# Optimization experiments

Hardware: AMD Instinct MI355X
Metric: run time of the kernel (lower is better)

## Reference

```python
import jax, jax.numpy as jnp
import numpy as np
import math

HEADS = 8


def rope(t):
    # t: [..., seq, dim]; lucidrains-style interleaved rotary embedding
    seq, dim = t.shape[-2], t.shape[-1]
    inv = 1.0 / (10000.0 ** (jnp.arange(0, dim, 2, dtype=jnp.float32) / dim))
    freqs = jnp.arange(seq, dtype=jnp.float32)[:, None] * inv[None, :]  # [seq, dim/2]
    freqs = jnp.repeat(freqs, 2, axis=-1)                               # [seq, dim]
    cos, sin = jnp.cos(freqs), jnp.sin(freqs)
    t2 = t.reshape(t.shape[:-1] + (dim // 2, 2))
    rot = jnp.stack([-t2[..., 1], t2[..., 0]], axis=-1).reshape(t.shape)
    return t * cos + rot * sin


def conv1x3(x, w):
    # x: [b,c,h,w], w: [out_c,in_c,1,3], padding (0,1), no bias
    return jax.lax.conv_general_dilated(
        x, w, window_strides=(1, 1), padding=((0, 0), (1, 1)),
        dimension_numbers=('NCHW', 'OIHW', 'NCHW'))


def mcl_pw(x, w_pw):
    # per-channel linear on feature axis h: w_pw [c, out_f, in_f]
    return jnp.einsum('bchw,cgh->bcgw', x, w_pw)


def setup_inputs() -> dict:
    key = jax.random.key(0)
    ks = jax.random.split(key, 10)
    b, c, f, w = 2, 8, 256, 1024
    s = 0.05
    return {
        'x': jax.random.normal(ks[0], (b, c, f, w), dtype=jnp.float32),
        'q_pw': jax.random.normal(ks[1], (c, f, f), dtype=jnp.float32) * s,
        'q_cw': jax.random.normal(ks[2], (c, c, 1, 3), dtype=jnp.float32) * s,
        'k_pw': jax.random.normal(ks[3], (c, f, f), dtype=jnp.float32) * s,
        'k_cw': jax.random.normal(ks[4], (c, c, 1, 3), dtype=jnp.float32) * s,
        'v_pw': jax.random.normal(ks[5], (c, f, f), dtype=jnp.float32) * s,
        'v_cw': jax.random.normal(ks[6], (c, c, 1, 3), dtype=jnp.float32) * s,
        'out_pw': jax.random.normal(ks[7], (c, f, f), dtype=jnp.float32) * s,
        'out_dw': jax.random.normal(ks[8], (c, c), dtype=jnp.float32) * s,
    }


def reference(x, q_pw, q_cw, k_pw, k_cw, v_pw, v_cw, out_pw, out_dw):
    b, c, h, w = x.shape
    hd = h // HEADS

    def split_heads(y):  # [b,c,h,w] -> [b,c,heads,w,hd]
        return y.transpose(0, 1, 3, 2).reshape(b, c, w, HEADS, hd).transpose(0, 1, 3, 2, 4)

    q = rope(split_heads(conv1x3(mcl_pw(x, q_pw), q_cw)))
    k = rope(split_heads(conv1x3(mcl_pw(x, k_pw), k_cw)))
    v = split_heads(conv1x3(mcl_pw(x, v_pw), v_cw))

    # non-standard scaling by sqrt(h) = sqrt(features)
    qk = jnp.einsum('bcnqd,bcnkd->bcnqk', q, k) / math.sqrt(h)
    a = jnp.einsum('bcnqk,bcnkd->bcnqd', jax.nn.softmax(qk, axis=-1), v)
    a = a.transpose(0, 1, 3, 2, 4).reshape(b, c, w, h).transpose(0, 1, 3, 2)  # [b,c,h,w]

    # out_proj: depthwise channel mix then per-channel positionwise linear
    out = jnp.einsum('bchw,dc->bdhw', a, out_dw)
    out = mcl_pw(out, out_pw)
    return out
```

## Files before the change

### kernel.cpp

```cpp
#include <hip/hip_runtime.h>
#include <hip/hip_bf16.h>

#define B 2
#define C 8
#define F 256
#define W 1024
#define NH 8
#define HD 32

typedef float f32x4 __attribute__((ext_vector_type(4)));
typedef short sh8 __attribute__((ext_vector_type(8)));
typedef short sh4 __attribute__((ext_vector_type(4)));
typedef unsigned short u16;

#define QSCALE 0.09016843880556021f

static __device__ __forceinline__ float fexp2(float x) {
#if __has_builtin(__builtin_amdgcn_exp2f)
  return __builtin_amdgcn_exp2f(x);
#else
  return __expf(x * 0.69314718056f);
#endif
}

static __device__ __forceinline__ u16 f2b(float x) {
  union { __hip_bfloat16 h; u16 u; } v;
  v.h = __float2bfloat16(x);
  return v.u;
}
static __device__ __forceinline__ float b2f(u16 x) {
  union { unsigned int u; float f; } v;
  v.u = ((unsigned int)x) << 16;
  return v.f;
}
static __device__ __forceinline__ float ubits(unsigned int u) {
  union { unsigned int u; float f; } v;
  v.u = u;
  return v.f;
}

static __device__ __forceinline__ f32x4 mfma32(sh8 a, sh8 b, f32x4 c) {
  return __builtin_amdgcn_mfma_f32_16x16x32_bf16(a, b, c, 0, 0, 0);
}

static __device__ __forceinline__ f32x4 mfma16(sh4 a, sh4 b, f32x4 c) {
#if __has_builtin(__builtin_amdgcn_mfma_f32_16x16x16bf16_1k)
  return __builtin_amdgcn_mfma_f32_16x16x16bf16_1k(a, b, c, 0, 0, 0);
#else
  f32x4 d;
  asm("v_mfma_f32_16x16x16_bf16 %0, %1, %2, %3" : "=v"(d) : "v"(a), "v"(b), "v"(c));
  return d;
#endif
}

static __device__ __forceinline__ void gload16(const u16* g, u16* l, int ln) {
#if __has_builtin(__builtin_amdgcn_global_load_lds)
  __builtin_amdgcn_global_load_lds((const __attribute__((address_space(1))) void*)g,
                                   (__attribute__((address_space(3))) void*)l, 16, 0, 0);
#else
  *(sh8*)(l + ln * 8) = *(const sh8*)g;
#endif
}

__global__ __launch_bounds__(256) void cvt4(const float* __restrict__ s0, const float* __restrict__ s1,
                                            const float* __restrict__ s2, const float* __restrict__ s3,
                                            u16* __restrict__ d0, u16* __restrict__ d1,
                                            u16* __restrict__ d2, u16* __restrict__ d3, int n4) {
  const int which = blockIdx.y;
  const float* s = which == 0 ? s0 : which == 1 ? s1 : which == 2 ? s2 : s3;
  u16* d = which == 0 ? d0 : which == 1 ? d1 : which == 2 ? d2 : d3;
  const int i = blockIdx.x * 256 + threadIdx.x;
  if (i < n4) {
    const float4 v = reinterpret_cast<const float4*>(s)[i];
    union { u16 h[4]; uint2 u; } o;
    o.h[0] = f2b(v.x); o.h[1] = f2b(v.y); o.h[2] = f2b(v.z); o.h[3] = f2b(v.w);
    reinterpret_cast<uint2*>(d)[i] = o.u;
  }
}

__global__ __launch_bounds__(256) void rope_tab_k(float2* __restrict__ TAB) {
  const int idx = blockIdx.x * 256 + threadIdx.x;
  const int j = idx >> 10, w = idx & 1023;
  const float inv = powf(10000.f, -(float)(2 * j) / 32.f);
  float sn, cs;
  sincosf((float)w * inv, &sn, &cs);
  TAB[idx] = make_float2(cs, sn);
}

__global__ __launch_bounds__(256) void xt_k(const float* __restrict__ x,
                                            u16* __restrict__ xt) {
  const int bc = blockIdx.z, h0 = blockIdx.y * 32, w0 = blockIdx.x * 32;
  const int t = threadIdx.x;
  __shared__ u16 sm[32][34];
  const int a = t & 31, bql = t >> 5;
  const float* src = x + ((size_t)bc * F + h0) * W + w0;
#pragma unroll
  for (int p = 0; p < 4; ++p) {
    const int hl = bql + p * 8;
    sm[a][hl] = f2b(src[(size_t)hl * W + a]);
  }
  __syncthreads();
  u16* dst = xt + ((size_t)bc * W + w0) * F + h0;
#pragma unroll
  for (int p = 0; p < 4; ++p) {
    const int wl = bql + p * 8;
    dst[(size_t)wl * F + a] = sm[wl][a];
  }
}

template <bool OUTBF>
__global__ __launch_bounds__(256) void gemm_bt(const u16* __restrict__ Aw,
                                               const u16* __restrict__ Bt,
                                               void* __restrict__ Cc) {
  const int bc = blockIdx.z;
  const int proj = blockIdx.y >> 1;
  const int g0 = (blockIdx.y & 1) * 128;
  const int w0 = blockIdx.x * 64;
  const int t = threadIdx.x;
  const int ln = t & 63, wid = t >> 6;
  const int lr = ln & 15, lk = (ln >> 4) * 8;
  const int wr = wid >> 1, wc = wid & 1;

  const u16* Ab = Aw + (size_t)proj * C * F * F + (size_t)(bc & 7) * F * F;
  const u16* Bb = Bt + (size_t)bc * W * F;

  __shared__ u16 sA[16 * 512];
  __shared__ u16 sB[8 * 512];

  const u16* ga0 = Ab + (size_t)(g0 + (wid * 2 + 0) * 16 + lr) * F + lk;
  const u16* ga1 = Ab + (size_t)(g0 + (wid * 2 + 1) * 16 + lr) * F + lk;
  const u16* gb0 = Bb + (size_t)(w0 + wid * 16 + lr) * F + lk;

  f32x4 acc[4][2] = {};

  for (int h0 = 0; h0 < F; h0 += 64) {
    __syncthreads();
    gload16(ga0 + h0,      &sA[(0 * 8 + wid * 2 + 0) * 512], ln);
    gload16(ga0 + h0 + 32, &sA[(1 * 8 + wid * 2 + 0) * 512], ln);
    gload16(ga1 + h0,      &sA[(0 * 8 + wid * 2 + 1) * 512], ln);
    gload16(ga1 + h0 + 32, &sA[(1 * 8 + wid * 2 + 1) * 512], ln);
    gload16(gb0 + h0,      &sB[(0 * 4 + wid) * 512], ln);
    gload16(gb0 + h0 + 32, &sB[(1 * 4 + wid) * 512], ln);
    __syncthreads();
#pragma unroll
    for (int kh = 0; kh < 2; ++kh) {
      sh8 af[4], bfr[2];
#pragma unroll
      for (int mi = 0; mi < 4; ++mi)
        af[mi] = *(const sh8*)&sA[((kh * 8 + wr * 4 + mi) * 64 + ln) * 8];
#pragma unroll
      for (int ni = 0; ni < 2; ++ni)
        bfr[ni] = *(const sh8*)&sB[((kh * 4 + wc * 2 + ni) * 64 + ln) * 8];
#pragma unroll
      for (int mi = 0; mi < 4; ++mi)
#pragma unroll
        for (int ni = 0; ni < 2; ++ni)
          acc[mi][ni] = mfma32(af[mi], bfr[ni], acc[mi][ni]);
    }
  }

  const int lq = ln >> 4;
  const size_t cbase = ((size_t)proj * B * C + bc) * F * W;
  if (OUTBF) {
    u16* Cb = (u16*)Cc + cbase;
#pragma unroll
    for (int mi = 0; mi < 4; ++mi)
#pragma unroll
      for (int ni = 0; ni < 2; ++ni)
#pragma unroll
        for (int r = 0; r < 4; ++r)
          Cb[(size_t)(g0 + wr * 64 + mi * 16 + lq * 4 + r) * W + w0 + wc * 32 + ni * 16 + lr] =
              f2b(acc[mi][ni][r]);
  } else {
    float* Cb = (float*)Cc + cbase;
#pragma unroll
    for (int mi = 0; mi < 4; ++mi)
#pragma unroll
      for (int ni = 0; ni < 2; ++ni)
#pragma unroll
        for (int r = 0; r < 4; ++r)
          Cb[(size_t)(g0 + wr * 64 + mi * 16 + lq * 4 + r) * W + w0 + wc * 32 + ni * 16 + lr] =
              acc[mi][ni][r];
  }
}

__global__ __launch_bounds__(256) void conv2(const u16* __restrict__ IN,
                                             const float* __restrict__ CWq,
                                             const float* __restrict__ CWk,
                                             const float* __restrict__ CWv,
                                             const float* __restrict__ TAB,
                                             u16* __restrict__ OUT) {
  const int f2 = blockIdx.x;
  const int z = blockIdx.y;
  const int proj = z >> 1, b = z & 1;
  const float* CW = proj == 0 ? CWq : proj == 1 ? CWk : CWv;
  const size_t NB = (size_t)B * C * F * W;
  const u16* INp = IN + (size_t)proj * NB;
  u16* OUTp = OUT + (size_t)proj * NB;
  const int do_rope = (proj < 2);
  const float scale = (proj == 0) ? QSCALE : 1.0f;
  const int f0 = f2 * 2;
  const int t = threadIdx.x;

  __shared__ u16 s[2][C][1040];
  __shared__ float cw[C][C][3];
  if (t < C * C * 3) ((float*)cw)[t] = CW[t];
  if (t < 16) {
    const int fi = t >> 3, c2 = t & 7;
    s[fi][c2][7] = 0;
    s[fi][c2][1032] = 0;
  }
  {
    const int l = t & 127, rsel = t >> 7;
#pragma unroll
    for (int p = 0; p < 8; ++p) {
      const int row = p * 2 + rsel;
      const int fi = row >> 3, c2 = row & 7;
      const u16* src = INp + ((size_t)(b * C + c2) * F + f0 + fi) * W + l * 8;
      *(sh8*)&s[fi][c2][8 + l * 8] = *(const sh8*)src;
    }
  }
  __syncthreads();

  float acc[2][C][4] = {};
#pragma unroll
  for (int c = 0; c < C; ++c) {
    float v[2][6];
#pragma unroll
    for (int fi = 0; fi < 2; ++fi) {
      const unsigned int* r32 = (const unsigned int*)&s[fi][c][0];
      const unsigned int r0 = r32[2 * t + 3];
      const unsigned int r1 = r32[2 * t + 4];
      const unsigned int r2 = r32[2 * t + 5];
      const unsigned int r3 = r32[2 * t + 6];
      v[fi][0] = ubits(r0 & 0xffff0000u);
      v[fi][1] = ubits(r1 << 16);
      v[fi][2] = ubits(r1 & 0xffff0000u);
      v[fi][3] = ubits(r2 << 16);
      v[fi][4] = ubits(r2 & 0xffff0000u);
      v[fi][5] = ubits(r3 << 16);
    }
#pragma unroll
    for (int d = 0; d < C; ++d) {
      const float c0 = cw[d][c][0], c1 = cw[d][c][1], c2_ = cw[d][c][2];
#pragma unroll
      for (int fi = 0; fi < 2; ++fi)
#pragma unroll
        for (int o = 0; o < 4; ++o)
          acc[fi][d][o] += v[fi][o] * c0 + v[fi][o + 1] * c1 + v[fi][o + 2] * c2_;
    }
  }

  float cs[4] = {1.f, 1.f, 1.f, 1.f}, sn[4] = {0.f, 0.f, 0.f, 0.f};
  if (do_rope) {
    const int j = f2 & 15;
    const float4* tp = (const float4*)(TAB + (size_t)(j * 1024 + 4 * t) * 2);
    const float4 A0 = tp[0], A1 = tp[1];
    cs[0] = A0.x; sn[0] = A0.y; cs[1] = A0.z; sn[1] = A0.w;
    cs[2] = A1.x; sn[2] = A1.y; cs[3] = A1.z; sn[3] = A1.w;
  }

#pragma unroll
  for (int d = 0; d < C; ++d) {
    sh4 pk0, pk1;
#pragma unroll
    for (int o = 0; o < 4; ++o) {
      const float a0 = acc[0][d][o], a1 = acc[1][d][o];
      float o0 = a0, o1 = a1;
      if (do_rope) { o0 = a0 * cs[o] - a1 * sn[o]; o1 = a1 * cs[o] + a0 * sn[o]; }
      pk0[o] = (short)f2b(o0 * scale);
      pk1[o] = (short)f2b(o1 * scale);
    }
    u16* dst = OUTp + ((size_t)(b * C + d) * F + f0) * W + 4 * t;
    *(sh4*)dst = pk0;
    *(sh4*)(dst + W) = pk1;
  }
}

__global__ __launch_bounds__(256) void attn_bf(const u16* __restrict__ Q,
                                               const u16* __restrict__ K,
                                               const u16* __restrict__ Vv,
                                               float* __restrict__ O) {
  const int bc = blockIdx.z, n = blockIdx.y, q0 = blockIdx.x * 64;
  const int t = threadIdx.x, ln = t & 63, wid = t >> 6;
  const int lc = ln & 15, g4 = (ln >> 4) * 4;
  const int dq = (ln >> 4) * 8;
  const size_t base = ((size_t)bc * F + n * HD) * W;

  __shared__ u16 Kl[2][64 * 40];
  __shared__ u16 Vl[2][32 * 76];

  const int sk = t & 63, sdb = (t >> 6) * 8;
  const int sd = t >> 3, skc = (t & 7) * 8;
  const u16* gK = K + base + (size_t)sdb * W + sk;
  const u16* gV = Vv + base + (size_t)sd * W + skc;

  const int qw = q0 + wid * 16 + lc;
  sh8 qf;
#pragma unroll
  for (int j = 0; j < 8; ++j) qf[j] = (short)Q[base + (size_t)(dq + j) * W + qw];

  f32x4 o0 = {0.f, 0.f, 0.f, 0.f}, o1 = {0.f, 0.f, 0.f, 0.f};
  float ls[4] = {0.f, 0.f, 0.f, 0.f};

  {
    sh8 hv;
#pragma unroll
    for (int j = 0; j < 8; ++j) hv[j] = (short)gK[(size_t)j * W];
    *(sh8*)&Kl[0][sk * 40 + sdb] = hv;
    *(sh8*)&Vl[0][sd * 76 + skc] = *(const sh8*)gV;
  }
  __syncthreads();

  for (int tile = 0; tile < 16; ++tile) {
    const int cur = tile & 1;
    sh8 hvK, hvV;
    if (tile < 15) {
      const int off = (tile + 1) * 64;
#pragma unroll
      for (int j = 0; j < 8; ++j) hvK[j] = (short)gK[(size_t)j * W + off];
      hvV = *(const sh8*)(gV + off);
    }

    f32x4 sf[4];
    __builtin_amdgcn_s_setprio(1);
#pragma unroll
    for (int kh = 0; kh < 4; ++kh) {
      const sh8 kf = *(const sh8*)&Kl[cur][(kh * 16 + lc) * 40 + dq];
      f32x4 z = {0.f, 0.f, 0.f, 0.f};
      sf[kh] = mfma32(kf, qf, z);
    }
    __builtin_amdgcn_s_setprio(0);

#pragma unroll
    for (int kh = 0; kh < 4; ++kh) {
      const float p0 = fexp2(sf[kh][0]);
      const float p1 = fexp2(sf[kh][1]);
      const float p2 = fexp2(sf[kh][2]);
      const float p3 = fexp2(sf[kh][3]);
      sf[kh][0] = p0; sf[kh][1] = p1; sf[kh][2] = p2; sf[kh][3] = p3;
      ls[kh] += (p0 + p1) + (p2 + p3);
    }

    __builtin_amdgcn_s_setprio(1);
#pragma unroll
    for (int kh = 0; kh < 4; ++kh) {
      const sh4 pb = {(short)f2b(sf[kh][0]), (short)f2b(sf[kh][1]),
                      (short)f2b(sf[kh][2]), (short)f2b(sf[kh][3])};
      const sh4 vf0 = *(const sh4*)&Vl[cur][lc * 76 + kh * 16 + g4];
      const sh4 vf1 = *(const sh4*)&Vl[cur][(16 + lc) * 76 + kh * 16 + g4];
      o0 = mfma16(pb, vf0, o0);
      o1 = mfma16(pb, vf1, o1);
    }
    __builtin_amdgcn_s_setprio(0);

    if (tile < 15) {
      *(sh8*)&Kl[cur ^ 1][sk * 40 + sdb] = hvK;
      *(sh8*)&Vl[cur ^ 1][sd * 76 + skc] = hvV;
    }
    __syncthreads();
  }

  float lsum = (ls[0] + ls[1]) + (ls[2] + ls[3]);
  lsum += __shfl_xor(lsum, 16);
  lsum += __shfl_xor(lsum, 32);
#pragma unroll
  for (int r = 0; r < 4; ++r) {
    const float inv = 1.f / __shfl(lsum, g4 + r);
    const int qrow = q0 + wid * 16 + g4 + r;
    O[base + (size_t)lc * W + qrow] = o0[r] * inv;
    O[base + (size_t)(16 + lc) * W + qrow] = o1[r] * inv;
  }
}

__global__ __launch_bounds__(256) void chanmix_t(const float* __restrict__ A,
                                                 const float* __restrict__ DW,
                                                 u16* __restrict__ O1) {
  const int b = blockIdx.z, f0 = blockIdx.y * 32, w0 = blockIdx.x * 32;
  const int t = threadIdx.x;
  __shared__ u16 sm[C][32][34];
  float dwv[C][C];
#pragma unroll
  for (int d = 0; d < C; ++d)
#pragma unroll
    for (int c = 0; c < C; ++c) dwv[d][c] = DW[d * C + c];

  const int wl = t & 31, fs = t >> 5;
#pragma unroll
  for (int p = 0; p < 4; ++p) {
    const int fl = p * 8 + fs;
    float av[C];
#pragma unroll
    for (int c = 0; c < C; ++c)
      av[c] = A[((size_t)(b * C + c) * F + f0 + fl) * W + w0 + wl];
#pragma unroll
    for (int d = 0; d < C; ++d) {
      float s = 0.f;
#pragma unroll
      for (int c = 0; c < C; ++c) s += av[c] * dwv[d][c];
      sm[d][wl][fl] = f2b(s);
    }
  }
  __syncthreads();
  const int fl2 = t & 31, ws = t >> 5;
#pragma unroll
  for (int d = 0; d < C; ++d)
#pragma unroll
    for (int p = 0; p < 4; ++p) {
      const int wl2 = p * 8 + ws;
      O1[((size_t)(b * C + d) * W + w0 + wl2) * F + f0 + fl2] = sm[d][wl2][fl2];
    }
}

extern "C" void kernel_launch(void* const* d_in, const int* in_sizes, int n_in,
                              void* d_out, int out_size, void* d_ws, size_t ws_size,
                              hipStream_t stream) {
  const float* x      = (const float*)d_in[0];
  const float* q_pw   = (const float*)d_in[1];
  const float* q_cw   = (const float*)d_in[2];
  const float* k_pw   = (const float*)d_in[3];
  const float* k_cw   = (const float*)d_in[4];
  const float* v_pw   = (const float*)d_in[5];
  const float* v_cw   = (const float*)d_in[6];
  const float* out_pw = (const float*)d_in[7];
  const float* out_dw = (const float*)d_in[8];

  const size_t NB = (size_t)B * C * F * W;
  const size_t CFF = (size_t)C * F * F;

  u16* xt   = (u16*)d_ws;
  u16* wqkv = xt + NB;
  u16* wo   = wqkv + 3 * CFF;
  u16* t0b  = wo + CFF;
  u16* qkvb = t0b + 3 * NB;
  float* tab = (float*)(qkvb + 3 * NB);
  float* obuf = (float*)t0b;
  u16* o1t  = xt;

  cvt4<<<dim3((int)(CFF / 4 + 255) / 256, 4), 256, 0, stream>>>(
      q_pw, k_pw, v_pw, out_pw, wqkv, wqkv + CFF, wqkv + 2 * CFF, wo, (int)(CFF / 4));
  rope_tab_k<<<64, 256, 0, stream>>>((float2*)tab);
  xt_k<<<dim3(W / 32, F / 32, B * C), 256, 0, stream>>>(x, xt);

  gemm_bt<true><<<dim3(W / 64, 6, B * C), 256, 0, stream>>>(wqkv, xt, t0b);
  conv2<<<dim3(F / 2, 3 * B), 256, 0, stream>>>(t0b, q_cw, k_cw, v_cw, tab, qkvb);

  attn_bf<<<dim3(W / 64, NH, B * C), 256, 0, stream>>>(qkvb, qkvb + NB, qkvb + 2 * NB, obuf);

  chanmix_t<<<dim3(W / 32, F / 32, B), 256, 0, stream>>>(obuf, out_dw, o1t);
  gemm_bt<false><<<dim3(W / 64, 2, B * C), 256, 0, stream>>>(wo, o1t, d_out);
}
```

Measured before the change: 118.1 us.

## Merge prep kernels and widen attention blocks to 128 queries

The three preprocessing kernels (weight conversion, rope table, x transpose) become one launch that dispatches on block index, saving two kernel launches. The attention kernel moves to 512 threads covering 128 queries per block, so each K/V tile staged in shared memory is reused by twice as many waves, with per-thread loads halved to match. The softmax denominator is now computed by an extra MFMA against a vector of ones instead of scalar adds and cross-lane shuffles, and probabilities are packed to bf16 pairs. The risks are lower occupancy from the larger blocks, fewer blocks in the attention grid, and an extra MFMA per key chunk.

```diff
diff --git a/kernel.cpp b/kernel.cpp
--- a/kernel.cpp
+++ b/kernel.cpp
@@ -27,6 +27,12 @@
   union { __hip_bfloat16 h; u16 u; } v;
   v.h = __float2bfloat16(x);
   return v.u;
+}
+static __device__ __forceinline__ sh4 pack4(float p0, float p1, float p2, float p3) {
+  union { __hip_bfloat162 h2[2]; sh4 s; } u;
+  u.h2[0] = __float22bfloat162_rn(make_float2(p0, p1));
+  u.h2[1] = __float22bfloat162_rn(make_float2(p2, p3));
+  return u.s;
 }
 static __device__ __forceinline__ float b2f(u16 x) {
   union { unsigned int u; float f; } v;
@@ -62,49 +68,49 @@
 #endif
 }
 
-__global__ __launch_bounds__(256) void cvt4(const float* __restrict__ s0, const float* __restrict__ s1,
+__global__ __launch_bounds__(256) void prep(const float* __restrict__ x, u16* __restrict__ xt,
+                                            const float* __restrict__ s0, const float* __restrict__ s1,
                                             const float* __restrict__ s2, const float* __restrict__ s3,
                                             u16* __restrict__ d0, u16* __restrict__ d1,
-                                            u16* __restrict__ d2, u16* __restrict__ d3, int n4) {
-  const int which = blockIdx.y;
-  const float* s = which == 0 ? s0 : which == 1 ? s1 : which == 2 ? s2 : s3;
-  u16* d = which == 0 ? d0 : which == 1 ? d1 : which == 2 ? d2 : d3;
-  const int i = blockIdx.x * 256 + threadIdx.x;
-  if (i < n4) {
-    const float4 v = reinterpret_cast<const float4*>(s)[i];
+                                            u16* __restrict__ d2, u16* __restrict__ d3,
+                                            float2* __restrict__ TAB) {
+  const int bid = blockIdx.x;
+  const int t = threadIdx.x;
+  if (bid < 4096) {
+    const int bc = bid >> 8, rem = bid & 255;
+    const int h0 = ((rem >> 5) & 7) * 32, w0 = (rem & 31) * 32;
+    __shared__ u16 sm[32][34];
+    const int a = t & 31, bql = t >> 5;
+    const float* src = x + ((size_t)bc * F + h0) * W + w0;
+#pragma unroll
+    for (int p = 0; p < 4; ++p) {
+      const int hl = bql + p * 8;
+      sm[a][hl] = f2b(src[(size_t)hl * W + a]);
+    }
+    __syncthreads();
+    u16* dst = xt + ((size_t)bc * W + w0) * F + h0;
+#pragma unroll
+    for (int p = 0; p < 4; ++p) {
+      const int wl = bql + p * 8;
+      dst[(size_t)wl * F + a] = sm[wl][a];
+    }
+  } else if (bid < 6144) {
+    const int i = bid - 4096;
+    const int which = i >> 9;
+    const float* s = which == 0 ? s0 : which == 1 ? s1 : which == 2 ? s2 : s3;
+    u16* d = which == 0 ? d0 : which == 1 ? d1 : which == 2 ? d2 : d3;
+    const int idx = (i & 511) * 256 + t;
+    const float4 v = reinterpret_cast<const float4*>(s)[idx];
     union { u16 h[4]; uint2 u; } o;
     o.h[0] = f2b(v.x); o.h[1] = f2b(v.y); o.h[2] = f2b(v.z); o.h[3] = f2b(v.w);
-    reinterpret_cast<uint2*>(d)[i] = o.u;
-  }
-}
-
-__global__ __launch_bounds__(256) void rope_tab_k(float2* __restrict__ TAB) {
-  const int idx = blockIdx.x * 256 + threadIdx.x;
-  const int j = idx >> 10, w = idx & 1023;
-  const float inv = powf(10000.f, -(float)(2 * j) / 32.f);
-  float sn, cs;
-  sincosf((float)w * inv, &sn, &cs);
-  TAB[idx] = make_float2(cs, sn);
-}
-
-__global__ __launch_bounds__(256) void xt_k(const float* __restrict__ x,
-                                            u16* __restrict__ xt) {
-  const int bc = blockIdx.z, h0 = blockIdx.y * 32, w0 = blockIdx.x * 32;
-  const int t = threadIdx.x;
-  __shared__ u16 sm[32][34];
-  const int a = t & 31, bql = t >> 5;
-  const float* src = x + ((size_t)bc * F + h0) * W + w0;
-#pragma unroll
-  for (int p = 0; p < 4; ++p) {
-    const int hl = bql + p * 8;
-    sm[a][hl] = f2b(src[(size_t)hl * W + a]);
-  }
-  __syncthreads();
-  u16* dst = xt + ((size_t)bc * W + w0) * F + h0;
-#pragma unroll
-  for (int p = 0; p < 4; ++p) {
-    const int wl = bql + p * 8;
-    dst[(size_t)wl * F + a] = sm[wl][a];
+    reinterpret_cast<uint2*>(d)[idx] = o.u;
+  } else {
+    const int idx = (bid - 6144) * 256 + t;
+    const int j = idx >> 10, w = idx & 1023;
+    const float inv = powf(10000.f, -(float)(2 * j) / 32.f);
+    float sn, cs;
+    sincosf((float)w * inv, &sn, &cs);
+    TAB[idx] = make_float2(cs, sn);
   }
 }
 
@@ -277,11 +283,11 @@
   }
 }
 
-__global__ __launch_bounds__(256) void attn_bf(const u16* __restrict__ Q,
+__global__ __launch_bounds__(512) void attn_bf(const u16* __restrict__ Q,
                                                const u16* __restrict__ K,
                                                const u16* __restrict__ Vv,
                                                float* __restrict__ O) {
-  const int bc = blockIdx.z, n = blockIdx.y, q0 = blockIdx.x * 64;
+  const int bc = blockIdx.z, n = blockIdx.y, q0 = blockIdx.x * 128;
   const int t = threadIdx.x, ln = t & 63, wid = t >> 6;
   const int lc = ln & 15, g4 = (ln >> 4) * 4;
   const int dq = (ln >> 4) * 8;
@@ -290,36 +296,37 @@
   __shared__ u16 Kl[2][64 * 40];
   __shared__ u16 Vl[2][32 * 76];
 
-  const int sk = t & 63, sdb = (t >> 6) * 8;
-  const int sd = t >> 3, skc = (t & 7) * 8;
-  const u16* gK = K + base + (size_t)sdb * W + sk;
-  const u16* gV = Vv + base + (size_t)sd * W + skc;
+  const int skey = t & 63, dq4 = (t >> 6) * 4;
+  const u16* gK = K + base + (size_t)dq4 * W + skey;
+  const int sd = t >> 4, kc4 = (t & 15) * 4;
+  const u16* gV = Vv + base + (size_t)sd * W + kc4;
 
   const int qw = q0 + wid * 16 + lc;
   sh8 qf;
 #pragma unroll
   for (int j = 0; j < 8; ++j) qf[j] = (short)Q[base + (size_t)(dq + j) * W + qw];
 
+  const sh4 ones = {0x3F80, 0x3F80, 0x3F80, 0x3F80};
   f32x4 o0 = {0.f, 0.f, 0.f, 0.f}, o1 = {0.f, 0.f, 0.f, 0.f};
-  float ls[4] = {0.f, 0.f, 0.f, 0.f};
+  f32x4 dn = {0.f, 0.f, 0.f, 0.f};
 
   {
-    sh8 hv;
-#pragma unroll
-    for (int j = 0; j < 8; ++j) hv[j] = (short)gK[(size_t)j * W];
-    *(sh8*)&Kl[0][sk * 40 + sdb] = hv;
-    *(sh8*)&Vl[0][sd * 76 + skc] = *(const sh8*)gV;
+    sh4 hv;
+#pragma unroll
+    for (int j = 0; j < 4; ++j) hv[j] = (short)gK[(size_t)j * W];
+    *(sh4*)&Kl[0][skey * 40 + dq4] = hv;
+    *(sh4*)&Vl[0][sd * 76 + kc4] = *(const sh4*)gV;
   }
   __syncthreads();
 
   for (int tile = 0; tile < 16; ++tile) {
     const int cur = tile & 1;
-    sh8 hvK, hvV;
+    sh4 hvK, hvV;
     if (tile < 15) {
       const int off = (tile + 1) * 64;
 #pragma unroll
-      for (int j = 0; j < 8; ++j) hvK[j] = (short)gK[(size_t)j * W + off];
-      hvV = *(const sh8*)(gV + off);
+      for (int j = 0; j < 4; ++j) hvK[j] = (short)gK[(size_t)j * W + off];
+      hvV = *(const sh4*)(gV + off);
     }
 
     f32x4 sf[4];
@@ -332,41 +339,37 @@
     }
     __builtin_amdgcn_s_setprio(0);
 
+    sh4 pb[4];
 #pragma unroll
     for (int kh = 0; kh < 4; ++kh) {
       const float p0 = fexp2(sf[kh][0]);
       const float p1 = fexp2(sf[kh][1]);
       const float p2 = fexp2(sf[kh][2]);
       const float p3 = fexp2(sf[kh][3]);
-      sf[kh][0] = p0; sf[kh][1] = p1; sf[kh][2] = p2; sf[kh][3] = p3;
-      ls[kh] += (p0 + p1) + (p2 + p3);
+      pb[kh] = pack4(p0, p1, p2, p3);
     }
 
     __builtin_amdgcn_s_setprio(1);
 #pragma unroll
     for (int kh = 0; kh < 4; ++kh) {
-      const sh4 pb = {(short)f2b(sf[kh][0]), (short)f2b(sf[kh][1]),
-                      (short)f2b(sf[kh][2]), (short)f2b(sf[kh][3])};
       const sh4 vf0 = *(const sh4*)&Vl[cur][lc * 76 + kh * 16 + g4];
       const sh4 vf1 = *(const sh4*)&Vl[cur][(16 + lc) * 76 + kh * 16 + g4];
-      o0 = mfma16(pb, vf0, o0);
-      o1 = mfma16(pb, vf1, o1);
+      o0 = mfma16(pb[kh], vf0, o0);
+      o1 = mfma16(pb[kh], vf1, o1);
+      dn = mfma16(pb[kh], ones, dn);
     }
     __builtin_amdgcn_s_setprio(0);
 
     if (tile < 15) {
-      *(sh8*)&Kl[cur ^ 1][sk * 40 + sdb] = hvK;
-      *(sh8*)&Vl[cur ^ 1][sd * 76 + skc] = hvV;
+      *(sh4*)&Kl[cur ^ 1][skey * 40 + dq4] = hvK;
+      *(sh4*)&Vl[cur ^ 1][sd * 76 + kc4] = hvV;
     }
     __syncthreads();
   }
 
-  float lsum = (ls[0] + ls[1]) + (ls[2] + ls[3]);
-  lsum += __shfl_xor(lsum, 16);
-  lsum += __shfl_xor(lsum, 32);
 #pragma unroll
   for (int r = 0; r < 4; ++r) {
-    const float inv = 1.f / __shfl(lsum, g4 + r);
+    const float inv = 1.f / dn[r];
     const int qrow = q0 + wid * 16 + g4 + r;
     O[base + (size_t)lc * W + qrow] = o0[r] * inv;
     O[base + (size_t)(16 + lc) * W + qrow] = o1[r] * inv;
@@ -437,15 +440,13 @@
   float* obuf = (float*)t0b;
   u16* o1t  = xt;
 
-  cvt4<<<dim3((int)(CFF / 4 + 255) / 256, 4), 256, 0, stream>>>(
-      q_pw, k_pw, v_pw, out_pw, wqkv, wqkv + CFF, wqkv + 2 * CFF, wo, (int)(CFF / 4));
-  rope_tab_k<<<64, 256, 0, stream>>>((float2*)tab);
-  xt_k<<<dim3(W / 32, F / 32, B * C), 256, 0, stream>>>(x, xt);
+  prep<<<4096 + 2048 + 64, 256, 0, stream>>>(
+      x, xt, q_pw, k_pw, v_pw, out_pw, wqkv, wqkv + CFF, wqkv + 2 * CFF, wo, (float2*)tab);
 
   gemm_bt<true><<<dim3(W / 64, 6, B * C), 256, 0, stream>>>(wqkv, xt, t0b);
   conv2<<<dim3(F / 2, 3 * B), 256, 0, stream>>>(t0b, q_cw, k_cw, v_cw, tab, qkvb);
 
-  attn_bf<<<dim3(W / 64, NH, B * C), 256, 0, stream>>>(qkvb, qkvb + NB, qkvb + 2 * NB, obuf);
+  attn_bf<<<dim3(W / 128, NH, B * C), 512, 0, stream>>>(qkvb, qkvb + NB, qkvb + 2 * NB, obuf);
 
   chanmix_t<<<dim3(W / 32, F / 32, B), 256, 0, stream>>>(obuf, out_dw, o1t);
   gemm_bt<false><<<dim3(W / 64, 2, B * C), 256, 0, stream>>>(wo, o1t, d_out);
```

After: 106.6 us. 9.7% less time.
